# Kernel tuning notes

Hardware: AMD Instinct MI355X
Metric: run time of the kernel (lower is better)

Reference implementation:

```python
import jax, jax.numpy as jnp
import numpy as np

N = 50000          # nodes
E = 800000         # edges (before self-loops)
IN = 128           # in_dim
HID = 128          # hidden_dim
HEADS = 4
G = 256            # graphs in batch
EPS = 1e-5         # batchnorm eps
NEG_SLOPE = 0.2    # GATConv leaky_relu slope


def _gat_layer(x, src, dst, W, a_src, a_dst, bias, H, C, concat):
    """PyG-style GATConv (self-loops already appended to src/dst)."""
    n = x.shape[0]
    h = (x @ W).reshape(n, H, C)                       # [N,H,C]
    s_src = (h * a_src).sum(-1)                        # [N,H]
    s_dst = (h * a_dst).sum(-1)                        # [N,H]
    e = jax.nn.leaky_relu(s_src[src] + s_dst[dst], NEG_SLOPE)   # [E',H]
    m = jax.ops.segment_max(e, dst, num_segments=n)    # segment-wise softmax
    ex = jnp.exp(e - m[dst])
    den = jax.ops.segment_sum(ex, dst, num_segments=n)
    alpha = ex / den[dst]                              # [E',H]
    out = jax.ops.segment_sum(alpha[..., None] * h[src], dst, num_segments=n)  # [N,H,C]
    out = out.reshape(n, H * C) if concat else out.mean(axis=1)
    return out + bias


def _bn(x, gamma, beta):
    # PyG BatchNorm over nodes (training-mode batch statistics)
    mu = x.mean(axis=0)
    var = x.var(axis=0)
    return gamma * (x - mu) * jax.lax.rsqrt(var + EPS) + beta


def setup_inputs() -> dict:
    key = jax.random.key(0)
    ks = jax.random.split(key, 32)
    d = {}
    d["x"] = jax.random.normal(ks[0], (N, IN), dtype=jnp.float32)
    d["edge_index"] = jax.random.randint(ks[1], (2, E), 0, N, dtype=jnp.int64)
    d["batch_idx"] = jnp.sort(jax.random.randint(ks[2], (N,), 0, G, dtype=jnp.int64))
    dims = [(IN, HEADS, HID, True), (HID * HEADS, HEADS, HID, True), (HID * HEADS, 1, HID, False)]
    for i, (din, H, C, concat) in enumerate(dims):
        d[f"W{i}"] = jax.random.normal(ks[3 + 4 * i], (din, H * C), dtype=jnp.float32) * 0.05
        d[f"att_src{i}"] = jax.random.normal(ks[4 + 4 * i], (H, C), dtype=jnp.float32) * 0.05
        d[f"att_dst{i}"] = jax.random.normal(ks[5 + 4 * i], (H, C), dtype=jnp.float32) * 0.05
        out_w = H * C if concat else C
        d[f"bias{i}"] = jnp.zeros((out_w,), dtype=jnp.float32)
        d[f"gamma{i}"] = jnp.ones((out_w,), dtype=jnp.float32)
        d[f"beta{i}"] = jnp.zeros((out_w,), dtype=jnp.float32)
    return d


def reference(x, edge_index, batch_idx,
              W0, att_src0, att_dst0, bias0, gamma0, beta0,
              W1, att_src1, att_dst1, bias1, gamma1, beta1,
              W2, att_src2, att_dst2, bias2, gamma2, beta2):
    n = x.shape[0]
    loops = jnp.arange(n, dtype=edge_index.dtype)
    src = jnp.concatenate([edge_index[0], loops])
    dst = jnp.concatenate([edge_index[1], loops])
    layers = [
        (W0, att_src0, att_dst0, bias0, gamma0, beta0, HEADS, HID, True),
        (W1, att_src1, att_dst1, bias1, gamma1, beta1, HEADS, HID, True),
        (W2, att_src2, att_dst2, bias2, gamma2, beta2, 1, HID, False),
    ]
    h = x
    for (W, a_s, a_d, b, g, bt, H, C, concat) in layers:
        h = _gat_layer(h, src, dst, W, a_s, a_d, b, H, C, concat)
        h = jax.nn.elu(_bn(h, g, bt))
        # dropout: identity in eval mode
    # global_mean_pool over batch_idx
    sums = jax.ops.segment_sum(h, batch_idx, num_segments=G)
    cnt = jax.ops.segment_sum(jnp.ones((n,), dtype=h.dtype), batch_idx, num_segments=G)
    return sums / jnp.maximum(cnt, 1.0)[:, None]
```

## Files before the change

kernel.cpp:

```cpp
#include <hip/hip_runtime.h>
#include <math.h>
#include <stdint.h>

#define N_NODES 50000
#define NPAD    50048
#define N_EDGES 800000
#define EP      (N_EDGES + N_NODES)
#define G_GRAPHS 256
#define BN_EPS   1e-5f
#define NEG_SLOPE 0.2f

typedef float f32x4 __attribute__((ext_vector_type(4)));
typedef _Float16 h16x8 __attribute__((ext_vector_type(8)));

static __device__ __forceinline__ float lrelu(float x) {
    return x > 0.f ? x : NEG_SLOPE * x;
}

static __device__ __forceinline__ void gld_lds16(const void* g, void* l) {
    __builtin_amdgcn_global_load_lds((const __attribute__((address_space(1))) void*)g,
                                     (__attribute__((address_space(3))) void*)l, 16, 0, 0);
}

static __device__ __forceinline__ float2 h2f2(unsigned u) {
    union { unsigned u; _Float16 h[2]; } c;
    c.u = u;
    return make_float2((float)c.h[0], (float)c.h[1]);
}

__global__ void k_hist(const int* __restrict__ ei, int* __restrict__ deg) {
    int stride = gridDim.x * blockDim.x;
    for (int e = blockIdx.x * blockDim.x + threadIdx.x; e < EP; e += stride) {
        int d = (e < N_EDGES) ? ei[N_EDGES + e] : (e - N_EDGES);
        atomicAdd(&deg[d], 1);
    }
}

__global__ void k_scan1(const int* __restrict__ deg, int* __restrict__ row_start,
                        int* __restrict__ totals) {
    __shared__ int buf[1024];
    int t = threadIdx.x;
    int i = blockIdx.x * 1024 + t;
    int v = (i < N_NODES) ? deg[i] : 0;
    buf[t] = v;
    __syncthreads();
    for (int off = 1; off < 1024; off <<= 1) {
        int add = (t >= off) ? buf[t - off] : 0;
        __syncthreads();
        buf[t] += add;
        __syncthreads();
    }
    if (i < N_NODES) row_start[i] = buf[t] - v;
    if (t == 1023) totals[blockIdx.x] = buf[t];
}

__global__ void k_scan2(int* __restrict__ totals, int nb) {
    if (threadIdx.x == 0 && blockIdx.x == 0) {
        int run = 0;
        for (int i = 0; i < nb; ++i) { int v = totals[i]; totals[i] = run; run += v; }
    }
}

__global__ void k_scan3(int* __restrict__ row_start, const int* __restrict__ totals) {
    int i = blockIdx.x * blockDim.x + threadIdx.x;
    if (i < N_NODES) row_start[i] += totals[i >> 10];
    if (i == 0) row_start[N_NODES] = EP;
}

__global__ void k_scatter(const int* __restrict__ ei, const int* __restrict__ row_start,
                          int* __restrict__ cursor, int* __restrict__ csr_src) {
    int stride = gridDim.x * blockDim.x;
    for (int e = blockIdx.x * blockDim.x + threadIdx.x; e < EP; e += stride) {
        int s, d;
        if (e < N_EDGES) { s = ei[e]; d = ei[N_EDGES + e]; }
        else             { s = d = e - N_EDGES; }
        int pos = row_start[d] + atomicAdd(&cursor[d], 1);
        csr_src[pos] = s;
    }
}

__global__ void k_cvtW(const float* __restrict__ W, _Float16* __restrict__ bthi,
                       int Nc, int nsh, int KS) {
    int i = blockIdx.x * 256 + threadIdx.x;
    if (i >= (KS << 5) * Nc) return;
    int k = i >> nsh;
    int n = i & (Nc - 1);
    int c = n >> 7, col = n & 127;
    int ks = k >> 5, kq = (k >> 3) & 3, j = k & 7;
    size_t idx = ((size_t)(c * KS + ks) << 12) + (kq << 10) + (col << 3) + j;
    bthi[idx] = (_Float16)W[i];
}

__global__ void k_bnprep(const float* __restrict__ bnsum, const float* __restrict__ bnsq,
                         const float* __restrict__ gamma, const float* __restrict__ beta,
                         float* __restrict__ scale, float* __restrict__ shift, int W) {
    int f = blockIdx.x * 256 + threadIdx.x;
    if (f >= W) return;
    const float invN = 1.f / (float)N_NODES;
    float mean = bnsum[f] * invN;
    float var  = bnsq[f] * invN - mean * mean;
    float sc = gamma[f] * rsqrtf(var + BN_EPS);
    scale[f] = sc;
    shift[f] = beta[f] - mean * sc;
}

__global__ void k_prepA0(const float* __restrict__ x, _Float16* __restrict__ Aswz,
                         int K, int s8, int KS) {
    int i = blockIdx.x * 256 + threadIdx.x;
    if (i >= NPAD * (K >> 3)) return;
    int r  = i >> s8;
    int c8 = i & ((K >> 3) - 1);
    int k  = c8 << 3;
    union { _Float16 h[8]; uint4 u; } pk;
    if (r < N_NODES) {
        float4 a0 = *(const float4*)&x[(size_t)r * K + k];
        float4 a1 = *(const float4*)&x[(size_t)r * K + k + 4];
        pk.h[0]=(_Float16)a0.x; pk.h[1]=(_Float16)a0.y; pk.h[2]=(_Float16)a0.z; pk.h[3]=(_Float16)a0.w;
        pk.h[4]=(_Float16)a1.x; pk.h[5]=(_Float16)a1.y; pk.h[6]=(_Float16)a1.z; pk.h[7]=(_Float16)a1.w;
    } else {
        pk.u.x = pk.u.y = pk.u.z = pk.u.w = 0u;
    }
    int rb = r >> 7, row = r & 127;
    int ks = k >> 5, kq = (k >> 3) & 3;
    size_t idx = ((size_t)(rb * KS + ks) << 12) + (kq << 10) + (row << 3);
    *(uint4*)&Aswz[idx] = pk.u;
}

__global__ void k_prepA1(const _Float16* __restrict__ act, const float* __restrict__ scale,
                         const float* __restrict__ shift, _Float16* __restrict__ Aswz,
                         int K, int s8, int KS) {
    int i = blockIdx.x * 256 + threadIdx.x;
    if (i >= NPAD * (K >> 3)) return;
    int r  = i >> s8;
    int c8 = i & ((K >> 3) - 1);
    int k  = c8 << 3;
    union { _Float16 h[8]; uint4 u; } pk;
    if (r < N_NODES) {
        uint4 v = *(const uint4*)&act[(size_t)r * K + k];
        float4 sc0 = *(const float4*)&scale[k];
        float4 sc1 = *(const float4*)&scale[k + 4];
        float4 sh0 = *(const float4*)&shift[k];
        float4 sh1 = *(const float4*)&shift[k + 4];
        float2 p0 = h2f2(v.x), p1 = h2f2(v.y), p2 = h2f2(v.z), p3 = h2f2(v.w);
        float y;
        y = fmaf(p0.x, sc0.x, sh0.x); pk.h[0] = (_Float16)(y > 0.f ? y : expm1f(y));
        y = fmaf(p0.y, sc0.y, sh0.y); pk.h[1] = (_Float16)(y > 0.f ? y : expm1f(y));
        y = fmaf(p1.x, sc0.z, sh0.z); pk.h[2] = (_Float16)(y > 0.f ? y : expm1f(y));
        y = fmaf(p1.y, sc0.w, sh0.w); pk.h[3] = (_Float16)(y > 0.f ? y : expm1f(y));
        y = fmaf(p2.x, sc1.x, sh1.x); pk.h[4] = (_Float16)(y > 0.f ? y : expm1f(y));
        y = fmaf(p2.y, sc1.y, sh1.y); pk.h[5] = (_Float16)(y > 0.f ? y : expm1f(y));
        y = fmaf(p3.x, sc1.z, sh1.z); pk.h[6] = (_Float16)(y > 0.f ? y : expm1f(y));
        y = fmaf(p3.y, sc1.w, sh1.w); pk.h[7] = (_Float16)(y > 0.f ? y : expm1f(y));
    } else {
        pk.u.x = pk.u.y = pk.u.z = pk.u.w = 0u;
    }
    int rb = r >> 7, row = r & 127;
    int ks = k >> 5, kq = (k >> 3) & 3;
    size_t idx = ((size_t)(rb * KS + ks) << 12) + (kq << 10) + (row << 3);
    *(uint4*)&Aswz[idx] = pk.u;
}

__launch_bounds__(256)
__global__ void k_gemm_f16(const _Float16* __restrict__ Aswz, const _Float16* __restrict__ bthi,
                           _Float16* __restrict__ C2,
                           float* __restrict__ sSg, float* __restrict__ sDg,
                           const float* __restrict__ asr, const float* __restrict__ adr,
                           int M, int K, int Nc) {
    __shared__ _Float16 Ah[2][4096], Bh[2][4096];
    __shared__ float rS[128], rD[128];
    const int t    = threadIdx.x;
    const int lane = t & 63, wv = t >> 6;
    const int wr = wv >> 1, wc = wv & 1;
    const int lr = lane & 15, kq = lane >> 4;
    const int r0 = blockIdx.x * 128, c0 = blockIdx.y * 128;
    const int KS = K >> 5;
    const int H = Nc >> 7;
    const int head = blockIdx.y;

    const size_t achunk0 = (size_t)blockIdx.x * KS * 4096;
    const size_t bchunk0 = (size_t)blockIdx.y * KS * 4096;
    const int ge0 = wv * 512 + lane * 8;
    const int le0 = wv * 512;

    f32x4 acc[4][4];
    #pragma unroll
    for (int m = 0; m < 4; ++m)
        #pragma unroll
        for (int n = 0; n < 4; ++n) {
            acc[m][n][0] = 0.f; acc[m][n][1] = 0.f;
            acc[m][n][2] = 0.f; acc[m][n][3] = 0.f;
        }

    {
        const _Float16* as  = Aswz + achunk0;
        const _Float16* bhs = bthi + bchunk0;
        #pragma unroll
        for (int p = 0; p < 2; ++p) {
            gld_lds16(as  + p * 2048 + ge0, &Ah[0][p * 2048 + le0]);
            gld_lds16(bhs + p * 2048 + ge0, &Bh[0][p * 2048 + le0]);
        }
    }

    for (int ks = 0; ks < KS; ++ks) {
        const int cur = ks & 1;
        if (ks + 1 < KS) {
            const _Float16* as  = Aswz + achunk0 + ((size_t)(ks + 1) << 12);
            const _Float16* bhs = bthi + bchunk0 + ((size_t)(ks + 1) << 12);
            #pragma unroll
            for (int p = 0; p < 2; ++p) {
                gld_lds16(as  + p * 2048 + ge0, &Ah[cur ^ 1][p * 2048 + le0]);
                gld_lds16(bhs + p * 2048 + ge0, &Bh[cur ^ 1][p * 2048 + le0]);
            }
            asm volatile("s_waitcnt vmcnt(4)" ::: "memory");
        } else {
            asm volatile("s_waitcnt vmcnt(0)" ::: "memory");
        }
        __builtin_amdgcn_s_barrier();

        h16x8 af[4], bfh[4];
        #pragma unroll
        for (int m = 0; m < 4; ++m) {
            int row = wr * 64 + m * 16 + lr;
            af[m] = *(const h16x8*)&Ah[cur][kq * 1024 + row * 8];
        }
        #pragma unroll
        for (int n = 0; n < 4; ++n) {
            int col = wc * 64 + n * 16 + lr;
            bfh[n] = *(const h16x8*)&Bh[cur][kq * 1024 + col * 8];
        }
        #pragma unroll
        for (int m = 0; m < 4; ++m)
            #pragma unroll
            for (int n = 0; n < 4; ++n)
                acc[m][n] = __builtin_amdgcn_mfma_f32_16x16x32_f16(af[m], bfh[n], acc[m][n], 0, 0, 0);

        asm volatile("s_waitcnt lgkmcnt(0)" ::: "memory");
        __builtin_amdgcn_s_barrier();
    }

    float aS[4], aD[4];
    #pragma unroll
    for (int n = 0; n < 4; ++n) {
        int c = c0 + wc * 64 + n * 16 + lr;
        aS[n] = asr[c];
        aD[n] = adr[c];
    }
    __syncthreads();
    if (t < 128) { rS[t] = 0.f; rD[t] = 0.f; }
    __syncthreads();
    #pragma unroll
    for (int m = 0; m < 4; ++m) {
        #pragma unroll
        for (int j = 0; j < 4; ++j) {
            float ps = 0.f, pd = 0.f;
            #pragma unroll
            for (int n = 0; n < 4; ++n) {
                float v = acc[m][n][j];
                ps += v * aS[n];
                pd += v * aD[n];
            }
            #pragma unroll
            for (int off = 1; off < 16; off <<= 1) {
                ps += __shfl_xor(ps, off, 64);
                pd += __shfl_xor(pd, off, 64);
            }
            if (lr == 0) {
                int row = wr * 64 + m * 16 + kq * 4 + j;
                atomicAdd(&rS[row], ps);
                atomicAdd(&rD[row], pd);
            }
        }
    }
    __syncthreads();
    if (t < 128) {
        int r = r0 + t;
        if (r < M) {
            sSg[(size_t)r * H + head] = rS[t];
            sDg[(size_t)r * H + head] = rD[t];
        }
    }

    #pragma unroll
    for (int m = 0; m < 4; ++m) {
        int rowb = r0 + wr * 64 + m * 16 + kq * 4;
        #pragma unroll
        for (int n = 0; n < 4; ++n) {
            int col = c0 + wc * 64 + n * 16 + lr;
            #pragma unroll
            for (int j = 0; j < 4; ++j) {
                int r = rowb + j;
                if (r < M) C2[(size_t)r * Nc + col] = (_Float16)acc[m][n][j];
            }
        }
    }
}

template<int H, int CPT, int CAP>
__launch_bounds__(256)
__global__ void k_attnagg(const _Float16* __restrict__ hb2, const float* __restrict__ s_src,
                          const float* __restrict__ s_dst, const int* __restrict__ row_start,
                          const int* __restrict__ csr, const float* __restrict__ bias,
                          _Float16* __restrict__ out) {
    const int W = H * 128;
    __shared__ float alds[4][CAP * H];
    const int wv = threadIdx.x >> 6;
    const int lane = threadIdx.x & 63;
    const int n = blockIdx.x * 4 + wv;
    if (n >= N_NODES) return;
    const int lo = row_start[n], hi = row_start[n + 1];
    const int deg = hi - lo;

    const int h1 = lane & (H - 1);
    const int eo = lane / H;
    const int EPI = 64 / H;
    float sd1 = s_dst[n * H + h1];
    const int c0 = lane * CPT;
    const int myh = c0 >> 7;
    float* al = &alds[wv][0];

    float acc[CPT];
    #pragma unroll
    for (int j = 0; j < CPT; ++j) acc[j] = 0.f;
    float invv;

    if (deg <= CAP) {
        float mx = -INFINITY;
        for (int q = eo; q < deg; q += EPI) {
            float e = lrelu(s_src[csr[lo + q] * H + h1] + sd1);
            al[q * H + h1] = e;
            mx = fmaxf(mx, e);
        }
        #pragma unroll
        for (int off = H; off < 64; off <<= 1) mx = fmaxf(mx, __shfl_xor(mx, off, 64));
        float sum = 0.f;
        for (int q = eo; q < deg; q += EPI) {
            float ex = expf(al[q * H + h1] - mx);
            al[q * H + h1] = ex;
            sum += ex;
        }
        #pragma unroll
        for (int off = H; off < 64; off <<= 1) sum += __shfl_xor(sum, off, 64);
        invv = __shfl(1.f / sum, myh, 64);
        asm volatile("s_waitcnt lgkmcnt(0)" ::: "memory");
        __builtin_amdgcn_sched_barrier(0);

        for (int q = 0; q < deg; q += 16) {
            int s[16];
            float a[16];
            #pragma unroll
            for (int j = 0; j < 16; ++j) {
                int qq = q + j;
                int qc = qq < deg ? qq : deg - 1;
                s[j] = csr[lo + qc];
                a[j] = (qq < deg) ? al[qc * H + myh] : 0.f;
            }
            if constexpr (CPT == 8) {
                uint4 v[16];
                #pragma unroll
                for (int j = 0; j < 16; ++j) v[j] = *(const uint4*)&hb2[(size_t)s[j] * W + c0];
                #pragma unroll
                for (int j = 0; j < 16; ++j) {
                    float2 x0 = h2f2(v[j].x), x1 = h2f2(v[j].y), x2 = h2f2(v[j].z), x3 = h2f2(v[j].w);
                    acc[0] += a[j]*x0.x; acc[1] += a[j]*x0.y; acc[2] += a[j]*x1.x; acc[3] += a[j]*x1.y;
                    acc[4] += a[j]*x2.x; acc[5] += a[j]*x2.y; acc[6] += a[j]*x3.x; acc[7] += a[j]*x3.y;
                }
            } else {
                unsigned v[16];
                #pragma unroll
                for (int j = 0; j < 16; ++j) v[j] = *(const unsigned*)&hb2[(size_t)s[j] * W + c0];
                #pragma unroll
                for (int j = 0; j < 16; ++j) {
                    float2 x = h2f2(v[j]);
                    acc[0] += a[j]*x.x; acc[1] += a[j]*x.y;
                }
            }
        }
    } else {
        float mx = -INFINITY;
        for (int p = lo + eo; p < hi; p += EPI) {
            float e = lrelu(s_src[csr[p] * H + h1] + sd1);
            mx = fmaxf(mx, e);
        }
        #pragma unroll
        for (int off = H; off < 64; off <<= 1) mx = fmaxf(mx, __shfl_xor(mx, off, 64));
        float sum = 0.f;
        for (int p = lo + eo; p < hi; p += EPI) {
            float e = lrelu(s_src[csr[p] * H + h1] + sd1);
            sum += expf(e - mx);
        }
        #pragma unroll
        for (int off = H; off < 64; off <<= 1) sum += __shfl_xor(sum, off, 64);
        float inv = 1.f / sum;
        float mxv = __shfl(mx, myh, 64);
        invv = __shfl(inv, myh, 64);
        float sdv = __shfl(sd1, myh, 64);
        for (int p = lo; p < hi; ++p) {
            int s0 = csr[p];
            float a0 = expf(lrelu(s_src[s0 * H + myh] + sdv) - mxv);
            if constexpr (CPT == 8) {
                uint4 v0 = *(const uint4*)&hb2[(size_t)s0 * W + c0];
                float2 x0 = h2f2(v0.x), x1 = h2f2(v0.y), x2 = h2f2(v0.z), x3 = h2f2(v0.w);
                acc[0] += a0*x0.x; acc[1] += a0*x0.y; acc[2] += a0*x1.x; acc[3] += a0*x1.y;
                acc[4] += a0*x2.x; acc[5] += a0*x2.y; acc[6] += a0*x3.x; acc[7] += a0*x3.y;
            } else {
                float2 x = h2f2(*(const unsigned*)&hb2[(size_t)s0 * W + c0]);
                acc[0] += a0*x.x; acc[1] += a0*x.y;
            }
        }
    }

    union { _Float16 h[CPT]; uint4 u4; unsigned u1; } pk;
    #pragma unroll
    for (int j = 0; j < CPT; ++j) pk.h[j] = (_Float16)(fmaf(acc[j], invv, bias[c0 + j]));
    if constexpr (CPT == 8)
        *(uint4*)&out[(size_t)n * W + c0] = pk.u4;
    else
        *(unsigned*)&out[(size_t)n * W + c0] = pk.u1;
}

__global__ void k_bnstat2(const _Float16* __restrict__ x, float* __restrict__ bnsum,
                          float* __restrict__ bnsq, int W) {
    const int RPB = 64;
    int t  = threadIdx.x;
    int r0 = blockIdx.x * RPB;
    int r1 = min(r0 + RPB, N_NODES);
    float s0 = 0.f, q0 = 0.f, s1 = 0.f, q1 = 0.f;
    for (int r = r0; r < r1; ++r) {
        float2 v = h2f2(*(const unsigned*)&x[(size_t)r * W + 2 * t]);
        s0 += v.x; q0 += v.x * v.x;
        s1 += v.y; q1 += v.y * v.y;
    }
    atomicAdd(&bnsum[2*t],   s0);
    atomicAdd(&bnsq[2*t],    q0);
    atomicAdd(&bnsum[2*t+1], s1);
    atomicAdd(&bnsq[2*t+1],  q1);
}

__global__ void k_pool(const _Float16* __restrict__ x, const int* __restrict__ batch,
                       const float* __restrict__ scale, const float* __restrict__ shift,
                       float* __restrict__ out) {
    int g = blockIdx.x;
    int f = threadIdx.x;
    int a = 0, b = N_NODES;
    while (a < b) { int m = (a + b) >> 1; if (batch[m] < g) a = m + 1; else b = m; }
    int lo = a;
    b = N_NODES;
    while (a < b) { int m = (a + b) >> 1; if (batch[m] < g + 1) a = m + 1; else b = m; }
    int hi = a;
    float sc = scale[f], sh = shift[f];
    float s = 0.f;
    for (int r = lo; r < hi; ++r) {
        float v = (float)x[(size_t)r * 128 + f];
        float y = fmaf(v, sc, sh);
        s += (y > 0.f) ? y : expm1f(y);
    }
    int cnt = hi - lo;
    out[g * 128 + f] = s / (float)(cnt > 0 ? cnt : 1);
}

extern "C" void kernel_launch(void* const* d_in, const int* in_sizes, int n_in,
                              void* d_out, int out_size, void* d_ws, size_t ws_size,
                              hipStream_t stream) {
    const float* x     = (const float*)d_in[0];
    const int*   ei    = (const int*)d_in[1];
    const int*   batch = (const int*)d_in[2];
    const float* Wm[3]  = {(const float*)d_in[3],  (const float*)d_in[9],  (const float*)d_in[15]};
    const float* asr[3] = {(const float*)d_in[4],  (const float*)d_in[10], (const float*)d_in[16]};
    const float* adr[3] = {(const float*)d_in[5],  (const float*)d_in[11], (const float*)d_in[17]};
    const float* bia[3] = {(const float*)d_in[6],  (const float*)d_in[12], (const float*)d_in[18]};
    const float* gam[3] = {(const float*)d_in[7],  (const float*)d_in[13], (const float*)d_in[19]};
    const float* bet[3] = {(const float*)d_in[8],  (const float*)d_in[14], (const float*)d_in[20]};

    char* w = (char*)d_ws;
    auto alloc = [&](size_t bytes) -> void* {
        void* p = (void*)w;
        w += (bytes + 255) & ~(size_t)255;
        return p;
    };
    _Float16* act2   = (_Float16*)alloc((size_t)N_NODES * 512 * 2);
    _Float16* act128 = (_Float16*)alloc((size_t)N_NODES * 128 * 2);
    _Float16* hb2    = (_Float16*)alloc((size_t)N_NODES * 512 * 2);
    _Float16* Aswz   = (_Float16*)alloc((size_t)NPAD * 512 * 2);
    int* csr_src   = (int*)alloc((size_t)EP * 4);
    int* row_start = (int*)alloc((size_t)(N_NODES + 1) * 4);
    int* deg       = (int*)alloc((size_t)N_NODES * 4);
    int* cursor    = (int*)alloc((size_t)N_NODES * 4);
    float* s_src = (float*)alloc((size_t)N_NODES * 4 * 4);
    float* s_dst = (float*)alloc((size_t)N_NODES * 4 * 4);
    float* bn    = (float*)alloc(1024 * 4);
    float* scl   = (float*)alloc(512 * 4);
    float* shf   = (float*)alloc(512 * 4);
    int* totals  = (int*)alloc(64 * 4);
    _Float16* bthi = (_Float16*)alloc((size_t)512 * 512 * 2);

    hipMemsetAsync(deg, 0, (size_t)N_NODES * 4, stream);
    hipMemsetAsync(cursor, 0, (size_t)N_NODES * 4, stream);
    k_hist<<<512, 256, 0, stream>>>(ei, deg);
    k_scan1<<<(N_NODES + 1023) / 1024, 1024, 0, stream>>>(deg, row_start, totals);
    k_scan2<<<1, 64, 0, stream>>>(totals, (N_NODES + 1023) / 1024);
    k_scan3<<<(N_NODES + 255) / 256, 256, 0, stream>>>(row_start, totals);
    k_scatter<<<512, 256, 0, stream>>>(ei, row_start, cursor, csr_src);

    auto layer = [&](int K, int li, int H, bool first, _Float16* outAct) {
        int Wd = H * 128;
        int nsh = (Wd == 512) ? 9 : 7;
        int KS = K >> 5;
        int s8 = (K == 512) ? 6 : 4;
        int tot = K * Wd;
        k_cvtW<<<(tot + 255) / 256, 256, 0, stream>>>(Wm[li], bthi, Wd, nsh, KS);
        int ptot = NPAD * (K >> 3);
        if (first)
            k_prepA0<<<(ptot + 255) / 256, 256, 0, stream>>>(x, Aswz, K, s8, KS);
        else
            k_prepA1<<<(ptot + 255) / 256, 256, 0, stream>>>(act2, scl, shf, Aswz, K, s8, KS);
        dim3 gg(NPAD / 128, Wd / 128);
        k_gemm_f16<<<gg, 256, 0, stream>>>(Aswz, bthi, hb2, s_src, s_dst,
                                           asr[li], adr[li], N_NODES, K, Wd);
        int nb = (N_NODES + 3) / 4;
        if (H == 4)
            k_attnagg<4, 8, 256><<<nb, 256, 0, stream>>>(hb2, s_src, s_dst, row_start, csr_src,
                                                         bia[li], outAct);
        else
            k_attnagg<1, 2, 256><<<nb, 256, 0, stream>>>(hb2, s_src, s_dst, row_start, csr_src,
                                                         bia[li], outAct);
        hipMemsetAsync(bn, 0, 1024 * 4, stream);
        k_bnstat2<<<(N_NODES + 63) / 64, Wd / 2, 0, stream>>>(outAct, bn, bn + 512, Wd);
        k_bnprep<<<(Wd + 255) / 256, 256, 0, stream>>>(bn, bn + 512, gam[li], bet[li], scl, shf, Wd);
    };

    layer(128, 0, 4, true,  act2);
    layer(512, 1, 4, false, act2);
    layer(512, 2, 1, false, act128);

    k_pool<<<G_GRAPHS, 128, 0, stream>>>(act128, batch, scl, shf, (float*)d_out);
}
```

Before: 844.1 us.

## Enlarge GEMM tile to 256 rows with 512-thread blocks for B reuse

The projection GEMM block now covers 256 rows instead of 128, using 8 waves, so each B tile loaded into LDS serves twice as many rows. Each wave still computes a 64x64 sub-tile, and NPAD is raised to a multiple of 256. The aim is to halve B-tile global traffic and the block count. In exchange each block needs more LDS and there are fewer blocks to fill the CUs. The load indexing (one 16-byte load per thread per chunk) appears consistent with the 512-thread layout.

```diff
diff --git a/kernel.cpp b/kernel.cpp
--- a/kernel.cpp
+++ b/kernel.cpp
@@ -3,7 +3,7 @@
 #include <stdint.h>
 
 #define N_NODES 50000
-#define NPAD    50048
+#define NPAD    50176
 #define N_EDGES 800000
 #define EP      (N_EDGES + N_NODES)
 #define G_GRAPHS 256
@@ -160,27 +160,28 @@
     *(uint4*)&Aswz[idx] = pk.u;
 }
 
-__launch_bounds__(256)
+__launch_bounds__(512)
 __global__ void k_gemm_f16(const _Float16* __restrict__ Aswz, const _Float16* __restrict__ bthi,
                            _Float16* __restrict__ C2,
                            float* __restrict__ sSg, float* __restrict__ sDg,
                            const float* __restrict__ asr, const float* __restrict__ adr,
                            int M, int K, int Nc) {
-    __shared__ _Float16 Ah[2][4096], Bh[2][4096];
-    __shared__ float rS[128], rD[128];
+    __shared__ _Float16 Ah[2][8192], Bh[2][4096];
+    __shared__ float rS[256], rD[256];
     const int t    = threadIdx.x;
     const int lane = t & 63, wv = t >> 6;
     const int wr = wv >> 1, wc = wv & 1;
     const int lr = lane & 15, kq = lane >> 4;
-    const int r0 = blockIdx.x * 128, c0 = blockIdx.y * 128;
+    const int r0 = blockIdx.x * 256, c0 = blockIdx.y * 128;
     const int KS = K >> 5;
     const int H = Nc >> 7;
     const int head = blockIdx.y;
 
-    const size_t achunk0 = (size_t)blockIdx.x * KS * 4096;
+    const size_t achunk0 = (size_t)(blockIdx.x * 2) * KS * 4096;
+    const size_t achunk1 = achunk0 + (size_t)KS * 4096;
     const size_t bchunk0 = (size_t)blockIdx.y * KS * 4096;
-    const int ge0 = wv * 512 + lane * 8;
-    const int le0 = wv * 512;
+    const int geo = wv * 512 + lane * 8;
+    const int leo = wv * 512;
 
     f32x4 acc[4][4];
     #pragma unroll
@@ -191,27 +192,18 @@
             acc[m][n][2] = 0.f; acc[m][n][3] = 0.f;
         }
 
-    {
-        const _Float16* as  = Aswz + achunk0;
-        const _Float16* bhs = bthi + bchunk0;
-        #pragma unroll
-        for (int p = 0; p < 2; ++p) {
-            gld_lds16(as  + p * 2048 + ge0, &Ah[0][p * 2048 + le0]);
-            gld_lds16(bhs + p * 2048 + ge0, &Bh[0][p * 2048 + le0]);
-        }
-    }
+    gld_lds16(Aswz + achunk0 + geo, &Ah[0][leo]);
+    gld_lds16(Aswz + achunk1 + geo, &Ah[0][4096 + leo]);
+    gld_lds16(bthi + bchunk0 + geo, &Bh[0][leo]);
 
     for (int ks = 0; ks < KS; ++ks) {
         const int cur = ks & 1;
         if (ks + 1 < KS) {
-            const _Float16* as  = Aswz + achunk0 + ((size_t)(ks + 1) << 12);
-            const _Float16* bhs = bthi + bchunk0 + ((size_t)(ks + 1) << 12);
-            #pragma unroll
-            for (int p = 0; p < 2; ++p) {
-                gld_lds16(as  + p * 2048 + ge0, &Ah[cur ^ 1][p * 2048 + le0]);
-                gld_lds16(bhs + p * 2048 + ge0, &Bh[cur ^ 1][p * 2048 + le0]);
-            }
-            asm volatile("s_waitcnt vmcnt(4)" ::: "memory");
+            const size_t off = (size_t)(ks + 1) << 12;
+            gld_lds16(Aswz + achunk0 + off + geo, &Ah[cur ^ 1][leo]);
+            gld_lds16(Aswz + achunk1 + off + geo, &Ah[cur ^ 1][4096 + leo]);
+            gld_lds16(bthi + bchunk0 + off + geo, &Bh[cur ^ 1][leo]);
+            asm volatile("s_waitcnt vmcnt(3)" ::: "memory");
         } else {
             asm volatile("s_waitcnt vmcnt(0)" ::: "memory");
         }
@@ -221,7 +213,8 @@
         #pragma unroll
         for (int m = 0; m < 4; ++m) {
             int row = wr * 64 + m * 16 + lr;
-            af[m] = *(const h16x8*)&Ah[cur][kq * 1024 + row * 8];
+            int ch = row >> 7, rr = row & 127;
+            af[m] = *(const h16x8*)&Ah[cur][ch * 4096 + kq * 1024 + rr * 8];
         }
         #pragma unroll
         for (int n = 0; n < 4; ++n) {
@@ -246,7 +239,7 @@
         aD[n] = adr[c];
     }
     __syncthreads();
-    if (t < 128) { rS[t] = 0.f; rD[t] = 0.f; }
+    if (t < 256) { rS[t] = 0.f; rD[t] = 0.f; }
     __syncthreads();
     #pragma unroll
     for (int m = 0; m < 4; ++m) {
@@ -272,7 +265,7 @@
         }
     }
     __syncthreads();
-    if (t < 128) {
+    if (t < 256) {
         int r = r0 + t;
         if (r < M) {
             sSg[(size_t)r * H + head] = rS[t];
@@ -513,8 +506,8 @@
             k_prepA0<<<(ptot + 255) / 256, 256, 0, stream>>>(x, Aswz, K, s8, KS);
         else
             k_prepA1<<<(ptot + 255) / 256, 256, 0, stream>>>(act2, scl, shf, Aswz, K, s8, KS);
-        dim3 gg(NPAD / 128, Wd / 128);
-        k_gemm_f16<<<gg, 256, 0, stream>>>(Aswz, bthi, hb2, s_src, s_dst,
+        dim3 gg(NPAD / 256, Wd / 128);
+        k_gemm_f16<<<gg, 512, 0, stream>>>(Aswz, bthi, hb2, s_src, s_dst,
                                            asr[li], adr[li], N_NODES, K, Wd);
         int nb = (N_NODES + 3) / 4;
         if (H == 4)
```

New measurement: 844.3 us. No clear change (+0.0%).
